# Performance work log

Measured on AMD Instinct MI355X. Metric: run time of the kernel, lower is better.

The kernel has to match this reference:

```python
import jax, jax.numpy as jnp
import numpy as np

B, S, V = 16, 256, 32000
E, H, L, FFN, NC = 256, 8, 2, 1024, 4
DK = E // H
NQ = E  # n_qubits == hidden_dim == embed_dim (required by the module's shape constraints)
EPS = 1e-5


def qproj(x, theta):
    # Analytic simulation of: RX(x_k) encode + trainable RX(theta_k) + CNOT ladder + MeasureAll(PauliZ).
    # RX gates on the same wire compose; CNOT ladder maps Z_j -> Z_0...Z_j in Heisenberg picture, so
    # <Z_j> = prod_{k<=j} cos(x_k + theta_k)  (product state expectation).
    return jnp.cumprod(jnp.cos(x + theta), axis=-1)


def layernorm(x, g, b):
    m = x.mean(-1, keepdims=True)
    v = x.var(-1, keepdims=True)
    return (x - m) * jax.lax.rsqrt(v + EPS) * g + b


def sinusoidal_pe(seq, d):
    pos = jnp.arange(seq, dtype=jnp.float32)[:, None]
    div = jnp.exp(jnp.arange(0, d, 2, dtype=jnp.float32) * (-np.log(10000.0) / d))
    pe = jnp.zeros((seq, d), jnp.float32)
    pe = pe.at[:, 0::2].set(jnp.sin(pos * div)).at[:, 1::2].set(jnp.cos(pos * div))
    return pe


def _forward(x, token_emb, lstm_W, lstm_b, lstm_theta, ln1_g, ln1_b, ln2_g, ln2_b,
             qkv_theta, combine_W, combine_b, ffn_theta, lin1_W, lin1_b, lin2_W, lin2_b,
             cls_W, cls_b):
    emb = token_emb[x]  # (B, S, E)

    # --- QLSTM: each gate = linear -> quantum circuit -> nonlinearity ---
    def step(carry, xt):
        hx, cx = carry
        comb = jnp.concatenate([xt, hx], axis=-1)                      # (B, 2E)
        z = jnp.einsum('bd,gdq->gbq', comb, lstm_W) + lstm_b[:, None]  # (4, B, NQ)
        q = jnp.cumprod(jnp.cos(z + lstm_theta[:, None, :]), axis=-1)
        f = jax.nn.sigmoid(q[0])
        i = jax.nn.sigmoid(q[1])
        g = jnp.tanh(q[2])
        o = jax.nn.sigmoid(q[3])
        cx = f * cx + i * g
        hx = o * jnp.tanh(cx)
        return (hx, cx), hx

    h0 = jnp.zeros((emb.shape[0], NQ), emb.dtype)
    _, hs = jax.lax.scan(step, (h0, h0), jnp.swapaxes(emb, 0, 1))
    h = jnp.swapaxes(hs, 0, 1)  # (B, S, NQ)

    h = h + sinusoidal_pe(h.shape[1], E)[None]

    # --- quantum transformer blocks ---
    def heads(t):
        return t.reshape(t.shape[0], t.shape[1], H, DK).transpose(0, 2, 1, 3)

    for l in range(L):
        q = qproj(h, qkv_theta[l, 0])
        k = qproj(h, qkv_theta[l, 1])
        v = qproj(h, qkv_theta[l, 2])
        qh, kh, vh = heads(q), heads(k), heads(v)
        scores = jnp.einsum('bhqd,bhkd->bhqk', qh, kh) / jnp.sqrt(jnp.float32(DK))
        attn = jax.nn.softmax(scores, axis=-1)
        out = jnp.einsum('bhqk,bhkd->bhqd', attn, vh).transpose(0, 2, 1, 3).reshape(h.shape)
        out = out @ combine_W[l] + combine_b[l]
        h = layernorm(h + out, ln1_g[l], ln1_b[l])
        ff = qproj(h, ffn_theta[l]) @ lin1_W[l] + lin1_b[l]
        ff = jax.nn.relu(ff) @ lin2_W[l] + lin2_b[l]
        h = layernorm(h + ff, ln2_g[l], ln2_b[l])

    pooled = h.mean(axis=1)  # (B, E)
    return pooled @ cls_W + cls_b  # (B, NC)


def setup_inputs() -> dict:
    key = jax.random.key(0)
    ks = jax.random.split(key, 10)
    s = 0.05
    return {
        'x': jax.random.randint(ks[0], (B, S), 0, V),
        'token_emb': jax.random.normal(ks[1], (V, E), jnp.float32) * s,
        'lstm_W': jax.random.normal(ks[2], (4, 2 * E, NQ), jnp.float32) * s,
        'lstm_b': jnp.zeros((4, NQ), jnp.float32),
        'lstm_theta': jax.random.normal(ks[3], (4, NQ), jnp.float32) * s,
        'ln1_g': jnp.ones((L, E), jnp.float32),
        'ln1_b': jnp.zeros((L, E), jnp.float32),
        'ln2_g': jnp.ones((L, E), jnp.float32),
        'ln2_b': jnp.zeros((L, E), jnp.float32),
        'qkv_theta': jax.random.normal(ks[4], (L, 3, E), jnp.float32) * s,
        'combine_W': jax.random.normal(ks[5], (L, E, E), jnp.float32) * s,
        'combine_b': jnp.zeros((L, E), jnp.float32),
        'ffn_theta': jax.random.normal(ks[6], (L, E), jnp.float32) * s,
        'lin1_W': jax.random.normal(ks[7], (L, E, FFN), jnp.float32) * s,
        'lin1_b': jnp.zeros((L, FFN), jnp.float32),
        'lin2_W': jax.random.normal(ks[8], (L, FFN, E), jnp.float32) * s,
        'lin2_b': jnp.zeros((L, E), jnp.float32),
        'cls_W': jax.random.normal(ks[9], (E, NC), jnp.float32) * s,
        'cls_b': jnp.zeros((NC,), jnp.float32),
    }


def reference(x, token_emb, lstm_W, lstm_b, lstm_theta, ln1_g, ln1_b, ln2_g, ln2_b,
              qkv_theta, combine_W, combine_b, ffn_theta, lin1_W, lin1_b, lin2_W, lin2_b,
              cls_W, cls_b):
    return _forward(x, token_emb, lstm_W, lstm_b, lstm_theta, ln1_g, ln1_b, ln2_g, ln2_b,
                    qkv_theta, combine_W, combine_b, ffn_theta, lin1_W, lin1_b, lin2_W, lin2_b,
                    cls_W, cls_b)
```

## Files before the change

### kernel.cpp

```cpp
#include <hip/hip_runtime.h>
#include <hip/hip_bf16.h>


typedef __attribute__((ext_vector_type(8))) short bf8v;
typedef __attribute__((ext_vector_type(4))) float f4v;
#define MFMA16 __builtin_amdgcn_mfma_f32_16x16x32_bf16

__device__ __forceinline__ unsigned short f2bf(float f) {
  unsigned u = __builtin_bit_cast(unsigned, f);
  u += 0x7fffu + ((u >> 16) & 1u);
  return (unsigned short)(u >> 16);
}
__device__ __forceinline__ float rcp_f(float x) { return __builtin_amdgcn_rcpf(x); }
__device__ __forceinline__ float sigm(float x) { return rcp_f(1.f + __expf(-x)); }
__device__ __forceinline__ float tanh_f(float x) { return 1.f - 2.f * rcp_f(__expf(2.f * x) + 1.f); }

#define DOT2BF(acc, a, b) \
  asm("v_dot2_f32_bf16 %0, %1, %2, %0" : "+v"(acc) : "v"(a), "v"(b))

__global__ void embed_kernel(const int* __restrict__ x, const float* __restrict__ tab,
                             unsigned short* __restrict__ eb) {
  int tok = blockIdx.x, tid = threadIdx.x;
  eb[tok * 256 + tid] = f2bf(tab[x[tok] * 256 + tid]);
}

__global__ void pack_bt(const float* __restrict__ W, int K, int N,
                        unsigned short* __restrict__ Th, long wz, long tz) {
  __shared__ float tile[64][65];
  W += (long)blockIdx.z * wz;
  Th += (long)blockIdx.z * tz;
  int n0 = blockIdx.x * 64, k0 = blockIdx.y * 64;
  int tid = threadIdx.x, tx = tid & 63, ty = tid >> 6;
  for (int r = ty; r < 64; r += 4) tile[r][tx] = W[(k0 + r) * N + n0 + tx];
  __syncthreads();
  for (int r = ty; r < 64; r += 4) {
    Th[(n0 + r) * K + k0 + tx] = f2bf(tile[tx][r]);
  }
}

__global__ void pack_wl_kernel(const float* __restrict__ lstmW, unsigned* __restrict__ WLg) {
  int gate = blockIdx.y;
  int o = blockIdx.x * 256 + threadIdx.x;
  int c = o & 3;
  int q = (o >> 2) & 255;
  int p4 = o >> 10;
  int d = 2 * (p4 * 4 + c);
  unsigned lo = f2bf(lstmW[(gate * 512 + 256 + d) * 256 + q]);
  unsigned hi = f2bf(lstmW[(gate * 512 + 256 + d + 1) * 256 + q]);
  WLg[gate * 32768 + o] = lo | (hi << 16);
}

__global__ void __launch_bounds__(256) gemm_mfma(const unsigned short* __restrict__ A,
                                                 const unsigned short* __restrict__ B,
                                                 const float* __restrict__ bias,
                                                 float* __restrict__ Cf,
                                                 unsigned short* __restrict__ Cb,
                                                 int M, int N, int K, int mode) {
  __shared__ unsigned short As[128 * 40];
  __shared__ unsigned short Bs[128 * 40];

  const int tid = threadIdx.x;
  const int lane = tid & 63;
  const int wid = tid >> 6;
  const int wr = wid >> 1, wc = wid & 1;
  const int bm = blockIdx.y * 128, bn = blockIdx.x * 128;

  const int srow = tid >> 2;
  const int scol = (tid & 3) * 8;

  f4v acc[4][4] = {};

  for (int kt = 0; kt < K; kt += 32) {
#pragma unroll
    for (int p = 0; p < 2; ++p) {
      int r = srow + p * 64;
      *(uint4*)(&As[r * 40 + scol]) = *(const uint4*)(&A[(bm + r) * K + kt + scol]);
      *(uint4*)(&Bs[r * 40 + scol]) = *(const uint4*)(&B[(bn + r) * K + kt + scol]);
    }
    __syncthreads();

    bf8v a[4], b[4];
    const int kq = (lane >> 4) * 8;
#pragma unroll
    for (int f = 0; f < 4; ++f) {
      a[f] = *(const bf8v*)(&As[(wr * 64 + f * 16 + (lane & 15)) * 40 + kq]);
      b[f] = *(const bf8v*)(&Bs[(wc * 64 + f * 16 + (lane & 15)) * 40 + kq]);
    }
#pragma unroll
    for (int fm = 0; fm < 4; ++fm)
#pragma unroll
      for (int fn = 0; fn < 4; ++fn)
        acc[fm][fn] = MFMA16(a[fm], b[fn], acc[fm][fn], 0, 0, 0);
    __syncthreads();
  }

#pragma unroll
  for (int fm = 0; fm < 4; ++fm)
#pragma unroll
    for (int fn = 0; fn < 4; ++fn) {
      int c = bn + wc * 64 + fn * 16 + (lane & 15);
      int r0 = bm + wr * 64 + fm * 16 + ((lane >> 4) << 2);
      float bv = bias[c];
#pragma unroll
      for (int j = 0; j < 4; ++j) {
        float v = acc[fm][fn][j] + bv;
        if (mode == 1) {
          Cb[(r0 + j) * N + c] = f2bf(fmaxf(v, 0.f));
        } else {
          Cf[(r0 + j) * N + c] = v;
        }
      }
    }
}

__global__ void __launch_bounds__(512)
lstm_kernel(const unsigned* __restrict__ WLgAll,
            const float* __restrict__ lstmTh,
            const float* __restrict__ xw,
            float* __restrict__ hb,
            unsigned long long* __restrict__ qex) {
  extern __shared__ char smem[];
  unsigned* WL = (unsigned*)smem;
  float* part = (float*)(smem + 131072);
  float* wtot = part + 512;
  unsigned* hp = (unsigned*)(wtot + 8);

  const int t = threadIdx.x;
  const int b = blockIdx.x >> 2;
  const int g = blockIdx.x & 3;
  const int q = t & 255;
  const int s = t >> 8;
  const int lane = t & 63;
  const int w = t >> 6;

  {
    const uint4* src = (const uint4*)WLgAll + g * 8192;
    uint4* dst = (uint4*)WL;
    for (int j = t; j < 8192; j += 512) dst[j] = src[j];
  }
  const float th = lstmTh[g * 256 + q];
  float cx = 0.f;
  if (t < 128) hp[t] = 0u;
  __syncthreads();

  const uint4* WL4 = (const uint4*)WL;
  const uint4* hp4 = (const uint4*)hp;
  const int xrow = (b << 8) * 1024 + g * 256 + q;

  for (int st = 0; st < 256; ++st) {
    float xv = xw[xrow + st * 1024];

    float acc = 0.f;
#pragma unroll
    for (int i4 = 0; i4 < 16; ++i4) {
      uint4 hh = hp4[(s << 4) + i4];
      uint4 wv = WL4[((s << 4) + i4) * 256 + q];
      DOT2BF(acc, wv.x, hh.x); DOT2BF(acc, wv.y, hh.y);
      DOT2BF(acc, wv.z, hh.z); DOT2BF(acc, wv.w, hh.w);
    }
    part[s * 256 + q] = acc;
    __syncthreads();

    float v = 0.f;
    if (t < 256) {
      float z = part[q] + part[256 + q] + xv + th;
      v = __cosf(z);
#pragma unroll
      for (int off = 1; off < 64; off <<= 1) {
        float o = __shfl_up(v, off, 64);
        if (lane >= off) v *= o;
      }
      if (lane == 63) wtot[w] = v;
    }
    __syncthreads();

    if (t < 256) {
      {
        float p = 1.f;
        int j = q >> 6;
        for (int k = 0; k < j; ++k) p *= wtot[k];
        v *= p;
      }
      const unsigned tag = (unsigned)(st + 1);
      const int par = st & 1;
      unsigned long long pk =
          ((unsigned long long)__builtin_bit_cast(unsigned, v) << 32) | tag;
      __hip_atomic_store(&qex[(((par * 16 + b) * 4 + g) << 8) + q], pk,
                         __ATOMIC_RELAXED, __HIP_MEMORY_SCOPE_AGENT);
      float q0v = 0.f, q1v = 0.f, q2v = 0.f, q3v = 0.f;
#pragma unroll
      for (int gg = 0; gg < 4; ++gg) {
        float val;
        if (gg == g) {
          val = v;
        } else {
          unsigned long long got;
          for (;;) {
            got = __hip_atomic_load(&qex[(((par * 16 + b) * 4 + gg) << 8) + q],
                                    __ATOMIC_RELAXED, __HIP_MEMORY_SCOPE_AGENT);
            if ((unsigned)got == tag) break;
            __builtin_amdgcn_s_sleep(1);
          }
          val = __builtin_bit_cast(float, (unsigned)(got >> 32));
        }
        if (gg == 0) q0v = val;
        else if (gg == 1) q1v = val;
        else if (gg == 2) q2v = val;
        else q3v = val;
      }
      float fg = sigm(q0v);
      float ig = sigm(q1v);
      float gg_ = tanh_f(q2v);
      float og = sigm(q3v);
      cx = fg * cx + ig * gg_;
      float hv = og * tanh_f(cx);
      if (g == 0) hb[((b << 8) + st) * 256 + q] = hv;
      float nb = __shfl_xor(hv, 1, 64);
      if ((t & 1) == 0) hp[t >> 1] = (unsigned)f2bf(hv) | ((unsigned)f2bf(nb) << 16);
    }
    __syncthreads();
  }
}

__global__ void pe_add_kernel(float* __restrict__ h) {
  int tok = blockIdx.x, tid = threadIdx.x;
  int s = tok & 255;
  int j = tid >> 1;
  float div = __expf((float)j * -0.07195578415622253f);
  float ang = (float)s * div;
  float pe = (tid & 1) ? __cosf(ang) : __sinf(ang);
  h[tok * 256 + tid] += pe;
}

__global__ void qproj3_kernel(const float* __restrict__ hin, const float* __restrict__ thetas,
                              float* __restrict__ outbase) {
  __shared__ float wtot[4];
  int tok = blockIdx.x, y = blockIdx.y;
  int tid = threadIdx.x, lane = tid & 63, wid = tid >> 6;
  const float* theta = thetas + y * 256;
  float* out = outbase + (long)y * 1048576;
  float v = __cosf(hin[tok * 256 + tid] + theta[tid]);
#pragma unroll
  for (int off = 1; off < 64; off <<= 1) {
    float o = __shfl_up(v, off, 64);
    if (lane >= off) v *= o;
  }
  if (lane == 63) wtot[wid] = v;
  __syncthreads();
  float pre = 1.f;
  for (int w = 0; w < wid; ++w) pre *= wtot[w];
  out[tok * 256 + tid] = v * pre;
}

__global__ void ln_qproj_kernel(float* __restrict__ hio, const float* __restrict__ delta,
                                const float* __restrict__ gamma, const float* __restrict__ beta,
                                const float* __restrict__ theta,
                                unsigned short* __restrict__ outb) {
  __shared__ float red[16];
  __shared__ float wtot[4];
  int tok = blockIdx.x, tid = threadIdx.x, lane = tid & 63, wid = tid >> 6;
  float v = hio[tok * 256 + tid] + delta[tok * 256 + tid];
  float s1 = v, s2 = v * v;
#pragma unroll
  for (int off = 32; off; off >>= 1) {
    s1 += __shfl_xor(s1, off, 64);
    s2 += __shfl_xor(s2, off, 64);
  }
  if (lane == 0) { red[wid] = s1; red[wid + 8] = s2; }
  __syncthreads();
  float t1 = red[0] + red[1] + red[2] + red[3];
  float t2 = red[8] + red[9] + red[10] + red[11];
  float mean = t1 * (1.f / 256.f);
  float var = t2 * (1.f / 256.f) - mean * mean;
  float w = rsqrtf(var + 1e-5f);
  float val = (v - mean) * w * gamma[tid] + beta[tid];
  hio[tok * 256 + tid] = val;
  float c = __cosf(val + theta[tid]);
#pragma unroll
  for (int off = 1; off < 64; off <<= 1) {
    float o = __shfl_up(c, off, 64);
    if (lane >= off) c *= o;
  }
  if (lane == 63) wtot[wid] = c;
  __syncthreads();
  float pre = 1.f;
  for (int k = 0; k < wid; ++k) pre *= wtot[k];
  outb[tok * 256 + tid] = f2bf(c * pre);
}

__global__ void __launch_bounds__(256, 1) attn_kernel(const float* __restrict__ qb,
                                                      const float* __restrict__ kb,
                                                      const float* __restrict__ vb,
                                                      unsigned short* __restrict__ outb) {
  extern __shared__ float sm[];
  float* Qs = sm;
  float* Ks = Qs + 256 * 36;
  float* Vs = Ks + 256 * 36;
  float* ps = Vs + 32 * 260;
  int hd = blockIdx.x, b = blockIdx.y;
  int tid = threadIdx.x, lane = tid & 63, wid = tid >> 6;
  const float scale = 0.17677669529663687f;

  for (int i = tid; i < 256 * 32; i += 256) {
    int r = i >> 5, d = i & 31;
    int src = (b * 256 + r) * 256 + hd * 32 + d;
    Qs[r * 36 + d] = qb[src];
    Ks[r * 36 + d] = kb[src];
    Vs[d * 260 + r] = vb[src];
  }
  __syncthreads();

  float* pw = ps + wid * 256;
  for (int r = wid; r < 256; r += 4) {
    float4 qreg[8];
    const float4* qrow = (const float4*)(Qs + r * 36);
#pragma unroll
    for (int i = 0; i < 8; ++i) qreg[i] = qrow[i];
    float s[4];
#pragma unroll
    for (int j = 0; j < 4; ++j) {
      int k = lane + 64 * j;
      const float4* kr = (const float4*)(Ks + k * 36);
      float a = 0.f;
#pragma unroll
      for (int i = 0; i < 8; ++i) {
        float4 kv = kr[i];
        a += qreg[i].x * kv.x + qreg[i].y * kv.y + qreg[i].z * kv.z + qreg[i].w * kv.w;
      }
      s[j] = a * scale;
    }
    float m = fmaxf(fmaxf(s[0], s[1]), fmaxf(s[2], s[3]));
#pragma unroll
    for (int off = 32; off; off >>= 1) m = fmaxf(m, __shfl_xor(m, off, 64));
    float p[4], sum = 0.f;
#pragma unroll
    for (int j = 0; j < 4; ++j) { p[j] = __expf(s[j] - m); sum += p[j]; }
#pragma unroll
    for (int off = 32; off; off >>= 1) sum += __shfl_xor(sum, off, 64);
    float inv = rcp_f(sum);
#pragma unroll
    for (int j = 0; j < 4; ++j) pw[lane + 64 * j] = p[j] * inv;
    int d = lane & 31, half = lane >> 5;
    const float4* pv = (const float4*)(pw + half * 128);
    const float4* v4 = (const float4*)(Vs + d * 260 + half * 128);
    float a = 0.f;
#pragma unroll
    for (int i = 0; i < 32; ++i) {
      float4 pp = pv[i];
      float4 vv = v4[i];
      a += pp.x * vv.x + pp.y * vv.y + pp.z * vv.z + pp.w * vv.w;
    }
    a += __shfl_down(a, 32, 64);
    if (lane < 32) outb[(b * 256 + r) * 256 + hd * 32 + d] = f2bf(a);
  }
}

__global__ void ln_kernel(float* __restrict__ hio, const float* __restrict__ delta,
                          const float* __restrict__ gamma, const float* __restrict__ beta) {
  __shared__ float red[16];
  int tok = blockIdx.x, tid = threadIdx.x, lane = tid & 63, wid = tid >> 6;
  float v = hio[tok * 256 + tid] + delta[tok * 256 + tid];
  float s1 = v, s2 = v * v;
#pragma unroll
  for (int off = 32; off; off >>= 1) {
    s1 += __shfl_xor(s1, off, 64);
    s2 += __shfl_xor(s2, off, 64);
  }
  if (lane == 0) { red[wid] = s1; red[wid + 8] = s2; }
  __syncthreads();
  float t1 = red[0] + red[1] + red[2] + red[3];
  float t2 = red[8] + red[9] + red[10] + red[11];
  float mean = t1 * (1.f / 256.f);
  float var = t2 * (1.f / 256.f) - mean * mean;
  float w = rsqrtf(var + 1e-5f);
  hio[tok * 256 + tid] = (v - mean) * w * gamma[tid] + beta[tid];
}

__global__ void pool_cls_kernel(const float* __restrict__ h, const float* __restrict__ clsW,
                                const float* __restrict__ clsb, float* __restrict__ out) {
  __shared__ float pl[256];
  __shared__ float red[8];
  int b = blockIdx.x, tid = threadIdx.x, lane = tid & 63, wid = tid >> 6;
  float s = 0.f;
  for (int t = 0; t < 256; ++t) s += h[(b * 256 + t) * 256 + tid];
  pl[tid] = s * (1.f / 256.f);
  __syncthreads();
  for (int c = 0; c < 4; ++c) {
    float v = pl[tid] * clsW[tid * 4 + c];
#pragma unroll
    for (int off = 32; off; off >>= 1) v += __shfl_xor(v, off, 64);
    if (lane == 0) red[wid] = v;
    __syncthreads();
    if (tid == 0) out[b * 4 + c] = red[0] + red[1] + red[2] + red[3] + clsb[c];
    __syncthreads();
  }
}

extern "C" void kernel_launch(void* const* d_in, const int* in_sizes, int n_in,
                              void* d_out, int out_size, void* d_ws, size_t ws_size,
                              hipStream_t stream) {
  const int* x = (const int*)d_in[0];
  const float* token_emb = (const float*)d_in[1];
  const float* lstm_W = (const float*)d_in[2];
  const float* lstm_b = (const float*)d_in[3];
  const float* lstm_th = (const float*)d_in[4];
  const float* ln1_g = (const float*)d_in[5];
  const float* ln1_b = (const float*)d_in[6];
  const float* ln2_g = (const float*)d_in[7];
  const float* ln2_b = (const float*)d_in[8];
  const float* qkv_th = (const float*)d_in[9];
  const float* comb_W = (const float*)d_in[10];
  const float* comb_b = (const float*)d_in[11];
  const float* ffn_th = (const float*)d_in[12];
  const float* lin1_W = (const float*)d_in[13];
  const float* lin1_b = (const float*)d_in[14];
  const float* lin2_W = (const float*)d_in[15];
  const float* lin2_b = (const float*)d_in[16];
  const float* cls_W = (const float*)d_in[17];
  const float* cls_b = (const float*)d_in[18];

  float* ws = (float*)d_ws;
  typedef unsigned short ushort_t;
  ushort_t* emb_b = (ushort_t*)ws;
  ushort_t* att_b = emb_b;
  float* xw = ws + 1048576;
  ushort_t* ffh_b = (ushort_t*)xw;
  float* hb = ws + 5242880;
  float* qq = ws + 6291456;
  float* kk = ws + 7340032;
  float* vv = ws + 8388608;
  float* tmp = ws + 9437184;
  unsigned* WLg = (unsigned*)tmp;
  ushort_t* ffq_b = (ushort_t*)(ws + 10485760);
  ushort_t* wxt_b = (ushort_t*)(ws + 11534336);
  ushort_t* cmb_b = wxt_b + 262144;
  ushort_t* l1_b = cmb_b + 131072;
  ushort_t* l2_b = l1_b + 524288;
  unsigned long long* qex = (unsigned long long*)(ws + 12255232);

  const int LSTM_LDS = 131072 + 2048 + 32 + 512;
  const int ATT_LDS = (256 * 36 * 2 + 32 * 260 + 4 * 256) * 4;
  (void)hipFuncSetAttribute(reinterpret_cast<const void*>(lstm_kernel),
                            hipFuncAttributeMaxDynamicSharedMemorySize, LSTM_LDS);
  (void)hipFuncSetAttribute(reinterpret_cast<const void*>(attn_kernel),
                            hipFuncAttributeMaxDynamicSharedMemorySize, ATT_LDS);

  hipMemsetAsync(qex, 0, 2 * 16 * 4 * 256 * 8, stream);

  embed_kernel<<<4096, 256, 0, stream>>>(x, token_emb, emb_b);
  pack_wl_kernel<<<dim3(128, 4), 256, 0, stream>>>(lstm_W, WLg);
  pack_bt<<<dim3(4, 4, 4), 256, 0, stream>>>(lstm_W, 256, 256, wxt_b, 131072, 65536);
  pack_bt<<<dim3(4, 4, 2), 256, 0, stream>>>(comb_W, 256, 256, cmb_b, 65536, 65536);
  pack_bt<<<dim3(16, 4, 2), 256, 0, stream>>>(lin1_W, 256, 1024, l1_b, 262144, 262144);
  pack_bt<<<dim3(4, 16, 2), 256, 0, stream>>>(lin2_W, 1024, 256, l2_b, 262144, 262144);

  gemm_mfma<<<dim3(8, 32), 256, 0, stream>>>(emb_b, wxt_b, lstm_b,
                                             xw, nullptr, 4096, 1024, 256, 0);
  lstm_kernel<<<64, 512, LSTM_LDS, stream>>>(WLg, lstm_th, xw, hb, qex);
  pe_add_kernel<<<4096, 256, 0, stream>>>(hb);

  for (int l = 0; l < 2; ++l) {
    qproj3_kernel<<<dim3(4096, 3), 256, 0, stream>>>(hb, qkv_th + l * 768, qq);
    attn_kernel<<<dim3(8, 16), 256, ATT_LDS, stream>>>(qq, kk, vv, att_b);
    gemm_mfma<<<dim3(2, 32), 256, 0, stream>>>(att_b, cmb_b + l * 65536, comb_b + l * 256,
                                               tmp, nullptr, 4096, 256, 256, 0);
    ln_qproj_kernel<<<4096, 256, 0, stream>>>(hb, tmp, ln1_g + l * 256, ln1_b + l * 256,
                                              ffn_th + l * 256, ffq_b);
    gemm_mfma<<<dim3(8, 32), 256, 0, stream>>>(ffq_b, l1_b + l * 262144, lin1_b + l * 1024,
                                               nullptr, ffh_b, 4096, 1024, 256, 1);
    gemm_mfma<<<dim3(2, 32), 256, 0, stream>>>(ffh_b, l2_b + l * 262144, lin2_b + l * 256,
                                               tmp, nullptr, 4096, 256, 1024, 0);
    ln_kernel<<<4096, 256, 0, stream>>>(hb, tmp, ln2_g + l * 256, ln2_b + l * 256);
  }

  pool_cls_kernel<<<16, 256, 0, stream>>>(hb, cls_W, cls_b, (float*)d_out);
}
```

Measured before the change: 1.192 ms.

## Use flag-based LSTM gate exchange, fuse PE add, smaller-tile GEMMs, split pooling

The LSTM cross-block exchange switches from per-element tagged 64-bit polling to 32-bit value stores plus one release flag per block, with a single wavefront spinning on the peer flags. The sinusoidal positional encoding is folded into the LSTM output write, which removes a separate kernel. The N=256 GEMMs move to a new 64x64-tile MFMA kernel so more workgroups are launched. Pooling is split into a parallel partial-sum pass and a final reduction. The flag path relies on release ordering of relaxed value stores, with extra block barriers per step.

```diff
diff --git a/kernel.cpp b/kernel.cpp
--- a/kernel.cpp
+++ b/kernel.cpp
@@ -113,12 +113,57 @@
     }
 }
 
+__global__ void __launch_bounds__(256) gemm64(const unsigned short* __restrict__ A,
+                                              const unsigned short* __restrict__ B,
+                                              const float* __restrict__ bias,
+                                              float* __restrict__ Cf,
+                                              int M, int N, int K) {
+  __shared__ unsigned short As[64 * 40];
+  __shared__ unsigned short Bs[64 * 40];
+
+  const int tid = threadIdx.x;
+  const int lane = tid & 63;
+  const int wid = tid >> 6;
+  const int bm = blockIdx.y * 64, bn = blockIdx.x * 64;
+  const int srow = tid >> 2;
+  const int scol = (tid & 3) * 8;
+
+  f4v acc[4] = {};
+
+  for (int kt = 0; kt < K; kt += 32) {
+    *(uint4*)(&As[srow * 40 + scol]) = *(const uint4*)(&A[(bm + srow) * K + kt + scol]);
+    *(uint4*)(&Bs[srow * 40 + scol]) = *(const uint4*)(&B[(bn + srow) * K + kt + scol]);
+    __syncthreads();
+
+    const int kq = (lane >> 4) * 8;
+    bf8v a = *(const bf8v*)(&As[(wid * 16 + (lane & 15)) * 40 + kq]);
+#pragma unroll
+    for (int f = 0; f < 4; ++f) {
+      bf8v b = *(const bf8v*)(&Bs[(f * 16 + (lane & 15)) * 40 + kq]);
+      acc[f] = MFMA16(a, b, acc[f], 0, 0, 0);
+    }
+    __syncthreads();
+  }
+
+#pragma unroll
+  for (int f = 0; f < 4; ++f) {
+    int c = bn + f * 16 + (lane & 15);
+    int r0 = bm + wid * 16 + ((lane >> 4) << 2);
+    float bv = bias[c];
+#pragma unroll
+    for (int j = 0; j < 4; ++j) {
+      Cf[(r0 + j) * N + c] = acc[f][j] + bv;
+    }
+  }
+}
+
 __global__ void __launch_bounds__(512)
 lstm_kernel(const unsigned* __restrict__ WLgAll,
             const float* __restrict__ lstmTh,
             const float* __restrict__ xw,
             float* __restrict__ hb,
-            unsigned long long* __restrict__ qex) {
+            unsigned* __restrict__ qv32,
+            unsigned* __restrict__ flg) {
   extern __shared__ char smem[];
   unsigned* WL = (unsigned*)smem;
   float* part = (float*)(smem + 131072);
@@ -149,6 +194,9 @@
 
   for (int st = 0; st < 256; ++st) {
     float xv = xw[xrow + st * 1024];
+    const int par = st & 1;
+    const int fbase = (par * 16 + b) * 4;
+    const unsigned tag = (unsigned)(st + 1);
 
     float acc = 0.f;
 #pragma unroll
@@ -175,61 +223,59 @@
     __syncthreads();
 
     if (t < 256) {
-      {
-        float p = 1.f;
-        int j = q >> 6;
-        for (int k = 0; k < j; ++k) p *= wtot[k];
-        v *= p;
-      }
-      const unsigned tag = (unsigned)(st + 1);
-      const int par = st & 1;
-      unsigned long long pk =
-          ((unsigned long long)__builtin_bit_cast(unsigned, v) << 32) | tag;
-      __hip_atomic_store(&qex[(((par * 16 + b) * 4 + g) << 8) + q], pk,
+      float p = 1.f;
+      int j = q >> 6;
+      for (int k = 0; k < j; ++k) p *= wtot[k];
+      v *= p;
+      __hip_atomic_store(&qv32[(fbase + g) * 256 + q],
+                         __builtin_bit_cast(unsigned, v),
                          __ATOMIC_RELAXED, __HIP_MEMORY_SCOPE_AGENT);
-      float q0v = 0.f, q1v = 0.f, q2v = 0.f, q3v = 0.f;
+    }
+    __syncthreads();
+
+    if (t >= 256 && t < 320) {
+      if (t == 256) {
+        __hip_atomic_store(&flg[fbase + g], tag, __ATOMIC_RELEASE,
+                           __HIP_MEMORY_SCOPE_AGENT);
+      }
+      int l = t - 256;
+      if (l < 3) {
+        int pg = (g + 1 + l) & 3;
+        while (__hip_atomic_load(&flg[fbase + pg], __ATOMIC_RELAXED,
+                                 __HIP_MEMORY_SCOPE_AGENT) < tag) {
+        }
+      }
+    }
+    __syncthreads();
+
+    if (t < 256) {
+      float gv[4];
 #pragma unroll
       for (int gg = 0; gg < 4; ++gg) {
-        float val;
         if (gg == g) {
-          val = v;
+          gv[gg] = v;
         } else {
-          unsigned long long got;
-          for (;;) {
-            got = __hip_atomic_load(&qex[(((par * 16 + b) * 4 + gg) << 8) + q],
-                                    __ATOMIC_RELAXED, __HIP_MEMORY_SCOPE_AGENT);
-            if ((unsigned)got == tag) break;
-            __builtin_amdgcn_s_sleep(1);
-          }
-          val = __builtin_bit_cast(float, (unsigned)(got >> 32));
+          unsigned u = __hip_atomic_load(&qv32[(fbase + gg) * 256 + q],
+                                         __ATOMIC_RELAXED, __HIP_MEMORY_SCOPE_AGENT);
+          gv[gg] = __builtin_bit_cast(float, u);
         }
-        if (gg == 0) q0v = val;
-        else if (gg == 1) q1v = val;
-        else if (gg == 2) q2v = val;
-        else q3v = val;
-      }
-      float fg = sigm(q0v);
-      float ig = sigm(q1v);
-      float gg_ = tanh_f(q2v);
-      float og = sigm(q3v);
+      }
+      float fg = sigm(gv[0]);
+      float ig = sigm(gv[1]);
+      float gg_ = tanh_f(gv[2]);
+      float og = sigm(gv[3]);
       cx = fg * cx + ig * gg_;
       float hv = og * tanh_f(cx);
-      if (g == 0) hb[((b << 8) + st) * 256 + q] = hv;
+      if (g == 0) {
+        float ang = (float)st * __expf((float)(q >> 1) * -0.07195578415622253f);
+        float pe = (q & 1) ? __cosf(ang) : __sinf(ang);
+        hb[((b << 8) + st) * 256 + q] = hv + pe;
+      }
       float nb = __shfl_xor(hv, 1, 64);
       if ((t & 1) == 0) hp[t >> 1] = (unsigned)f2bf(hv) | ((unsigned)f2bf(nb) << 16);
     }
     __syncthreads();
   }
-}
-
-__global__ void pe_add_kernel(float* __restrict__ h) {
-  int tok = blockIdx.x, tid = threadIdx.x;
-  int s = tok & 255;
-  int j = tid >> 1;
-  float div = __expf((float)j * -0.07195578415622253f);
-  float ang = (float)s * div;
-  float pe = (tid & 1) ? __cosf(ang) : __sinf(ang);
-  h[tok * 256 + tid] += pe;
 }
 
 __global__ void qproj3_kernel(const float* __restrict__ hin, const float* __restrict__ thetas,
@@ -376,13 +422,22 @@
   hio[tok * 256 + tid] = (v - mean) * w * gamma[tid] + beta[tid];
 }
 
-__global__ void pool_cls_kernel(const float* __restrict__ h, const float* __restrict__ clsW,
-                                const float* __restrict__ clsb, float* __restrict__ out) {
+__global__ void poolA_kernel(const float* __restrict__ h, float* __restrict__ partial) {
+  int bx = blockIdx.x;
+  int b = bx >> 4, ch = bx & 15;
+  int tid = threadIdx.x;
+  float s = 0.f;
+  for (int tt = ch * 16; tt < ch * 16 + 16; ++tt) s += h[((b << 8) + tt) * 256 + tid];
+  partial[bx * 256 + tid] = s;
+}
+
+__global__ void poolB_kernel(const float* __restrict__ partial, const float* __restrict__ clsW,
+                             const float* __restrict__ clsb, float* __restrict__ out) {
   __shared__ float pl[256];
   __shared__ float red[8];
   int b = blockIdx.x, tid = threadIdx.x, lane = tid & 63, wid = tid >> 6;
   float s = 0.f;
-  for (int t = 0; t < 256; ++t) s += h[(b * 256 + t) * 256 + tid];
+  for (int ch = 0; ch < 16; ++ch) s += partial[(b * 16 + ch) * 256 + tid];
   pl[tid] = s * (1.f / 256.f);
   __syncthreads();
   for (int c = 0; c < 4; ++c) {
@@ -436,7 +491,9 @@
   ushort_t* cmb_b = wxt_b + 262144;
   ushort_t* l1_b = cmb_b + 131072;
   ushort_t* l2_b = l1_b + 524288;
-  unsigned long long* qex = (unsigned long long*)(ws + 12255232);
+  unsigned* qv32 = (unsigned*)(ws + 12255232);
+  unsigned* flg = (unsigned*)(ws + 12287999 + 1);
+  float* partial = ws + 12288128;
 
   const int LSTM_LDS = 131072 + 2048 + 32 + 512;
   const int ATT_LDS = (256 * 36 * 2 + 32 * 260 + 4 * 256) * 4;
@@ -445,7 +502,7 @@
   (void)hipFuncSetAttribute(reinterpret_cast<const void*>(attn_kernel),
                             hipFuncAttributeMaxDynamicSharedMemorySize, ATT_LDS);
 
-  hipMemsetAsync(qex, 0, 2 * 16 * 4 * 256 * 8, stream);
+  hipMemsetAsync(flg, 0, 128 * 4, stream);
 
   embed_kernel<<<4096, 256, 0, stream>>>(x, token_emb, emb_b);
   pack_wl_kernel<<<dim3(128, 4), 256, 0, stream>>>(lstm_W, WLg);
@@ -456,22 +513,22 @@
 
   gemm_mfma<<<dim3(8, 32), 256, 0, stream>>>(emb_b, wxt_b, lstm_b,
                                              xw, nullptr, 4096, 1024, 256, 0);
-  lstm_kernel<<<64, 512, LSTM_LDS, stream>>>(WLg, lstm_th, xw, hb, qex);
-  pe_add_kernel<<<4096, 256, 0, stream>>>(hb);
+  lstm_kernel<<<64, 512, LSTM_LDS, stream>>>(WLg, lstm_th, xw, hb, qv32, flg);
 
   for (int l = 0; l < 2; ++l) {
     qproj3_kernel<<<dim3(4096, 3), 256, 0, stream>>>(hb, qkv_th + l * 768, qq);
     attn_kernel<<<dim3(8, 16), 256, ATT_LDS, stream>>>(qq, kk, vv, att_b);
-    gemm_mfma<<<dim3(2, 32), 256, 0, stream>>>(att_b, cmb_b + l * 65536, comb_b + l * 256,
-                                               tmp, nullptr, 4096, 256, 256, 0);
+    gemm64<<<dim3(4, 64), 256, 0, stream>>>(att_b, cmb_b + l * 65536, comb_b + l * 256,
+                                            tmp, 4096, 256, 256);
     ln_qproj_kernel<<<4096, 256, 0, stream>>>(hb, tmp, ln1_g + l * 256, ln1_b + l * 256,
                                               ffn_th + l * 256, ffq_b);
     gemm_mfma<<<dim3(8, 32), 256, 0, stream>>>(ffq_b, l1_b + l * 262144, lin1_b + l * 1024,
                                                nullptr, ffh_b, 4096, 1024, 256, 1);
-    gemm_mfma<<<dim3(2, 32), 256, 0, stream>>>(ffh_b, l2_b + l * 262144, lin2_b + l * 256,
-                                               tmp, nullptr, 4096, 256, 1024, 0);
+    gemm64<<<dim3(4, 64), 256, 0, stream>>>(ffh_b, l2_b + l * 262144, lin2_b + l * 256,
+                                            tmp, 4096, 256, 1024);
     ln_kernel<<<4096, 256, 0, stream>>>(hb, tmp, ln2_g + l * 256, ln2_b + l * 256);
   }
 
-  pool_cls_kernel<<<16, 256, 0, stream>>>(hb, cls_W, cls_b, (float*)d_out);
-}
+  poolA_kernel<<<256, 256, 0, stream>>>(hb, partial);
+  poolB_kernel<<<16, 256, 0, stream>>>(partial, cls_W, cls_b, (float*)d_out);
+}
```

Result: slower. 1.380 ms (+15.8%).
